# Kernel optimization log

Measured on AMD Instinct MI355X. Metric: run time of the kernel, lower is better.

## Reference

```python
import jax, jax.numpy as jnp
import numpy as np

NV = 6890   # SMPL vertex count (hard-coded in module)
NF = 13776  # SMPL face count
BATCH = 64


def _make_laplacian():
    # Mirrors LaplacianLoss.__init__: symmetric -1 adjacency from triangle
    # faces, diagonal = vertex degree, each row normalized by diag + 1e-8.
    rng = np.random.default_rng(0)
    faces = rng.integers(0, NV, size=(NF, 3))
    L = np.zeros((NV, NV), dtype=np.float32)
    L[faces[:, 0], faces[:, 1]] = -1
    L[faces[:, 1], faces[:, 0]] = -1
    L[faces[:, 1], faces[:, 2]] = -1
    L[faces[:, 2], faces[:, 1]] = -1
    L[faces[:, 2], faces[:, 0]] = -1
    L[faces[:, 0], faces[:, 2]] = -1
    r, c = np.diag_indices(NV)
    L[r, c] = -L.sum(1)
    L = L / (np.diag(L)[:, None] + 1e-8)
    return jnp.asarray(L)


def setup_inputs() -> dict:
    key = jax.random.key(0)
    x = jax.random.normal(key, (BATCH, NV, 3), dtype=jnp.float32)
    laplacian = _make_laplacian()
    return {"x": x, "laplacian": laplacian}


def reference(x, laplacian):
    # Dense Laplacian applied per batch: [v,w] x [b,w,d] -> [b,v,d]
    lx = jnp.einsum('vw,bwd->bvd', laplacian, x)
    # Squared norm over coordinate dim, then mean over (batch, vertices)
    # (average=False branch of the original module).
    return jnp.mean(jnp.sum(lx * lx, axis=2))
```

## Files before the change

kernel.cpp:

```cpp
#include <hip/hip_runtime.h>

#define NV    6890
#define NB    64
#define NCOL  192
#define CAP_W 256
#define MAIN4 1722
#define NIT   14
#define SCALE (1.0f / (64.0f * 6890.0f))

__global__ __launch_bounds__(256) void transpose_x_kernel(
    const float* __restrict__ x, float* __restrict__ Xt) {
  int i = blockIdx.x * blockDim.x + threadIdx.x;
  const int total = NB * NV * 3;
  if (i >= total) return;
  int d = i % 3;
  int w = (i / 3) % NV;
  int b = i / (3 * NV);
  Xt[(size_t)w * NCOL + b * 3 + d] = x[i];
}

template <bool USE_XT, bool USE_PARTIALS>
__global__ __launch_bounds__(256) void lap_rows_wave_kernel(
    const float* __restrict__ L,
    const float* __restrict__ X,
    float* __restrict__ partials,
    float* __restrict__ out_atomic) {
  const int lane = threadIdx.x & 63;
  const int wv   = threadIdx.x >> 6;
  const int v    = blockIdx.x * 4 + wv;
  if (v >= NV) return;

  __shared__ float4 s_c4[4][CAP_W];
  __shared__ int    s_cb[4][CAP_W];
  float4* __restrict__ sc4 = s_c4[wv];
  int*    __restrict__ scb = s_cb[wv];

  const float* __restrict__ row = L + (size_t)v * NV;
  const int head     = (v & 1) ? 2 : 0;
  const int extraPos = head ? 0 : (NV - 2);
  const float4* __restrict__ m4 = (const float4*)(row + head);

  const unsigned long long lmask = (1ull << lane) - 1ull;

  const int n0 = lane, n1 = lane + 64, n2 = lane + 128;
  const size_t o0 = (size_t)(n0 / 3) * (NV * 3) + (n0 % 3);
  const size_t o1 = (size_t)(n1 / 3) * (NV * 3) + (n1 % 3);
  const size_t o2 = (size_t)(n2 / 3) * (NV * 3) + (n2 % 3);

  float a0 = 0.f, a1 = 0.f, a2 = 0.f;
  int nnz = 0;

  auto gather3 = [&](float val, int col) {
    if (USE_XT) {
      const float* __restrict__ xr = X + (size_t)col * NCOL;
      a0 = fmaf(val, xr[n0], a0);
      a1 = fmaf(val, xr[n1], a1);
      a2 = fmaf(val, xr[n2], a2);
    } else {
      const size_t cb = (size_t)col * 3;
      a0 = fmaf(val, X[cb + o0], a0);
      a1 = fmaf(val, X[cb + o1], a1);
      a2 = fmaf(val, X[cb + o2], a2);
    }
  };

  auto apply = [&](int count) {
    for (int j = 0; j < count; ++j) {
      float4 f = sc4[j];
      int    cb = scb[j];
      if (f.x != 0.f) gather3(f.x, cb);
      if (f.y != 0.f) gather3(f.y, cb + 1);
      if (f.z != 0.f) gather3(f.z, cb + 2);
      if (f.w != 0.f) gather3(f.w, cb + 3);
    }
  };

  auto push_chunk = [&](bool nz, float4 f, int colbase) {
    unsigned long long m = __ballot(nz);
    if (nz) {
      int pos = nnz + __popcll(m & lmask);
      sc4[pos] = f;
      scb[pos] = colbase;
    }
    nnz += __popcll(m);
  };

  {
    const bool act = lane < 2;
    const int  col = extraPos + lane;
    float val = act ? row[col] : 0.f;
    push_chunk(val != 0.f, make_float4(val, 0.f, 0.f, 0.f), col);
  }

  for (int it = 0; it < NIT; ++it) {
    const int i0 = it * 128 + lane;
    const int i1 = i0 + 64;
    float4 f0 = make_float4(0.f, 0.f, 0.f, 0.f);
    float4 f1 = make_float4(0.f, 0.f, 0.f, 0.f);
    if (i0 < MAIN4) f0 = m4[i0];
    if (i1 < MAIN4) f1 = m4[i1];
    const bool nz0 = (f0.x != 0.f) | (f0.y != 0.f) | (f0.z != 0.f) | (f0.w != 0.f);
    const bool nz1 = (f1.x != 0.f) | (f1.y != 0.f) | (f1.z != 0.f) | (f1.w != 0.f);
    push_chunk(nz0, f0, head + i0 * 4);
    push_chunk(nz1, f1, head + i1 * 4);
    if (nnz > CAP_W - 130) { apply(nnz); nnz = 0; }
  }
  apply(nnz);

  float sq = fmaf(a0, a0, fmaf(a1, a1, a2 * a2));
  #pragma unroll
  for (int o = 32; o > 0; o >>= 1) sq += __shfl_down(sq, o);
  if (lane == 0) {
    if (USE_PARTIALS) partials[v] = sq;
    else              atomicAdd(out_atomic, sq * SCALE);
  }
}

__global__ __launch_bounds__(256) void reduce_kernel(
    const float* __restrict__ p, float* __restrict__ out) {
  int tid = threadIdx.x;
  float a = 0.0f;
  for (int i = tid; i < NV; i += 256) a += p[i];
  #pragma unroll
  for (int o = 32; o > 0; o >>= 1) a += __shfl_down(a, o);
  __shared__ float s_w[4];
  if ((tid & 63) == 0) s_w[tid >> 6] = a;
  __syncthreads();
  if (tid == 0) out[0] = (s_w[0] + s_w[1] + s_w[2] + s_w[3]) * SCALE;
}

__global__ void zero_out_kernel(float* p) {
  if (threadIdx.x == 0 && blockIdx.x == 0) p[0] = 0.0f;
}

extern "C" void kernel_launch(void* const* d_in, const int* in_sizes, int n_in,
                              void* d_out, int out_size, void* d_ws, size_t ws_size,
                              hipStream_t stream) {
  const float* x = (const float*)d_in[0];
  const float* L = (const float*)d_in[1];
  float* out = (float*)d_out;

  const size_t xt_bytes   = (size_t)NV * NCOL * sizeof(float);
  const size_t part_bytes = (size_t)NV * sizeof(float);
  const int grid = (NV + 3) / 4;

  if (ws_size >= xt_bytes + part_bytes) {
    float* Xt       = (float*)d_ws;
    float* partials = (float*)((char*)d_ws + xt_bytes);
    const int total = NB * NV * 3;
    transpose_x_kernel<<<(total + 255) / 256, 256, 0, stream>>>(x, Xt);
    lap_rows_wave_kernel<true, true><<<grid, 256, 0, stream>>>(L, Xt, partials, nullptr);
    reduce_kernel<<<1, 256, 0, stream>>>(partials, out);
  } else if (ws_size >= part_bytes) {
    float* partials = (float*)d_ws;
    lap_rows_wave_kernel<false, true><<<grid, 256, 0, stream>>>(L, x, partials, nullptr);
    reduce_kernel<<<1, 256, 0, stream>>>(partials, out);
  } else {
    zero_out_kernel<<<1, 64, 0, stream>>>(out);
    lap_rows_wave_kernel<false, false><<<grid, 256, 0, stream>>>(L, x, nullptr, out);
  }
}
```

Before: 63.04 us.

## Replace LDS nonzero compaction with ballot/readlane gathers and prefetch next row chunk

The per-wave shared-memory compaction of nonzero Laplacian entries is replaced by per-component ballots: each set bit is walked with ctz, and the value is broadcast with readlane before gathering the X row. The next float4 chunks of the row are software-prefetched one iteration ahead. The transpose kernel is reindexed so its writes are contiguous and its reads are gathered. This removes LDS traffic and the batch flush logic, but issues up to eight serialized ballot loops per iteration.

```diff
diff --git a/kernel.cpp b/kernel.cpp
--- a/kernel.cpp
+++ b/kernel.cpp
@@ -3,7 +3,6 @@
 #define NV    6890
 #define NB    64
 #define NCOL  192
-#define CAP_W 256
 #define MAIN4 1722
 #define NIT   14
 #define SCALE (1.0f / (64.0f * 6890.0f))
@@ -11,12 +10,13 @@
 __global__ __launch_bounds__(256) void transpose_x_kernel(
     const float* __restrict__ x, float* __restrict__ Xt) {
   int i = blockIdx.x * blockDim.x + threadIdx.x;
-  const int total = NB * NV * 3;
+  const int total = NV * NCOL;
   if (i >= total) return;
-  int d = i % 3;
-  int w = (i / 3) % NV;
-  int b = i / (3 * NV);
-  Xt[(size_t)w * NCOL + b * 3 + d] = x[i];
+  int n = i % NCOL;
+  int w = i / NCOL;
+  int b = n / 3;
+  int d = n % 3;
+  Xt[i] = x[(size_t)b * (NV * 3) + (size_t)w * 3 + d];
 }
 
 template <bool USE_XT, bool USE_PARTIALS>
@@ -30,17 +30,10 @@
   const int v    = blockIdx.x * 4 + wv;
   if (v >= NV) return;
 
-  __shared__ float4 s_c4[4][CAP_W];
-  __shared__ int    s_cb[4][CAP_W];
-  float4* __restrict__ sc4 = s_c4[wv];
-  int*    __restrict__ scb = s_cb[wv];
-
   const float* __restrict__ row = L + (size_t)v * NV;
   const int head     = (v & 1) ? 2 : 0;
   const int extraPos = head ? 0 : (NV - 2);
   const float4* __restrict__ m4 = (const float4*)(row + head);
-
-  const unsigned long long lmask = (1ull << lane) - 1ull;
 
   const int n0 = lane, n1 = lane + 64, n2 = lane + 128;
   const size_t o0 = (size_t)(n0 / 3) * (NV * 3) + (n0 % 3);
@@ -48,64 +41,69 @@
   const size_t o2 = (size_t)(n2 / 3) * (NV * 3) + (n2 % 3);
 
   float a0 = 0.f, a1 = 0.f, a2 = 0.f;
-  int nnz = 0;
 
-  auto gather3 = [&](float val, int col) {
-    if (USE_XT) {
-      const float* __restrict__ xr = X + (size_t)col * NCOL;
-      a0 = fmaf(val, xr[n0], a0);
-      a1 = fmaf(val, xr[n1], a1);
-      a2 = fmaf(val, xr[n2], a2);
-    } else {
-      const size_t cb = (size_t)col * 3;
-      a0 = fmaf(val, X[cb + o0], a0);
-      a1 = fmaf(val, X[cb + o1], a1);
-      a2 = fmaf(val, X[cb + o2], a2);
+  auto proc = [&](unsigned long long m, float src, int col0, int stride) {
+    while (m) {
+      const int s = (int)__builtin_ctzll(m);
+      m &= m - 1;
+      const float val =
+          __int_as_float(__builtin_amdgcn_readlane(__float_as_int(src), s));
+      const int col = col0 + s * stride;
+      if (USE_XT) {
+        const float* __restrict__ xr = X + (size_t)col * NCOL;
+        a0 = fmaf(val, xr[n0], a0);
+        a1 = fmaf(val, xr[n1], a1);
+        a2 = fmaf(val, xr[n2], a2);
+      } else {
+        const size_t cb = (size_t)col * 3;
+        a0 = fmaf(val, X[cb + o0], a0);
+        a1 = fmaf(val, X[cb + o1], a1);
+        a2 = fmaf(val, X[cb + o2], a2);
+      }
     }
-  };
-
-  auto apply = [&](int count) {
-    for (int j = 0; j < count; ++j) {
-      float4 f = sc4[j];
-      int    cb = scb[j];
-      if (f.x != 0.f) gather3(f.x, cb);
-      if (f.y != 0.f) gather3(f.y, cb + 1);
-      if (f.z != 0.f) gather3(f.z, cb + 2);
-      if (f.w != 0.f) gather3(f.w, cb + 3);
-    }
-  };
-
-  auto push_chunk = [&](bool nz, float4 f, int colbase) {
-    unsigned long long m = __ballot(nz);
-    if (nz) {
-      int pos = nnz + __popcll(m & lmask);
-      sc4[pos] = f;
-      scb[pos] = colbase;
-    }
-    nnz += __popcll(m);
   };
 
   {
     const bool act = lane < 2;
-    const int  col = extraPos + lane;
-    float val = act ? row[col] : 0.f;
-    push_chunk(val != 0.f, make_float4(val, 0.f, 0.f, 0.f), col);
+    const float val = act ? row[extraPos + lane] : 0.f;
+    proc(__ballot(act && val != 0.f), val, extraPos, 1);
   }
 
+  float4 c0 = m4[lane];
+  float4 c1 = m4[lane + 64];
   for (int it = 0; it < NIT; ++it) {
     const int i0 = it * 128 + lane;
     const int i1 = i0 + 64;
-    float4 f0 = make_float4(0.f, 0.f, 0.f, 0.f);
-    float4 f1 = make_float4(0.f, 0.f, 0.f, 0.f);
-    if (i0 < MAIN4) f0 = m4[i0];
-    if (i1 < MAIN4) f1 = m4[i1];
-    const bool nz0 = (f0.x != 0.f) | (f0.y != 0.f) | (f0.z != 0.f) | (f0.w != 0.f);
-    const bool nz1 = (f1.x != 0.f) | (f1.y != 0.f) | (f1.z != 0.f) | (f1.w != 0.f);
-    push_chunk(nz0, f0, head + i0 * 4);
-    push_chunk(nz1, f1, head + i1 * 4);
-    if (nnz > CAP_W - 130) { apply(nnz); nnz = 0; }
+    const int j0 = min(i0 + 128, MAIN4 - 1);
+    const int j1 = min(i1 + 128, MAIN4 - 1);
+    const float4 p0 = m4[j0];
+    const float4 p1 = m4[j1];
+
+    const bool act0 = i0 < MAIN4;
+    const bool act1 = i1 < MAIN4;
+    const unsigned long long mx0 = __ballot(act0 && c0.x != 0.f);
+    const unsigned long long my0 = __ballot(act0 && c0.y != 0.f);
+    const unsigned long long mz0 = __ballot(act0 && c0.z != 0.f);
+    const unsigned long long mw0 = __ballot(act0 && c0.w != 0.f);
+    const unsigned long long mx1 = __ballot(act1 && c1.x != 0.f);
+    const unsigned long long my1 = __ballot(act1 && c1.y != 0.f);
+    const unsigned long long mz1 = __ballot(act1 && c1.z != 0.f);
+    const unsigned long long mw1 = __ballot(act1 && c1.w != 0.f);
+
+    const int base0 = head + it * 512;
+    const int base1 = base0 + 256;
+    proc(mx0, c0.x, base0 + 0, 4);
+    proc(my0, c0.y, base0 + 1, 4);
+    proc(mz0, c0.z, base0 + 2, 4);
+    proc(mw0, c0.w, base0 + 3, 4);
+    proc(mx1, c1.x, base1 + 0, 4);
+    proc(my1, c1.y, base1 + 1, 4);
+    proc(mz1, c1.z, base1 + 2, 4);
+    proc(mw1, c1.w, base1 + 3, 4);
+
+    c0 = p0;
+    c1 = p1;
   }
-  apply(nnz);
 
   float sq = fmaf(a0, a0, fmaf(a1, a1, a2 * a2));
   #pragma unroll
@@ -147,7 +145,7 @@
   if (ws_size >= xt_bytes + part_bytes) {
     float* Xt       = (float*)d_ws;
     float* partials = (float*)((char*)d_ws + xt_bytes);
-    const int total = NB * NV * 3;
+    const int total = NV * NCOL;
     transpose_x_kernel<<<(total + 255) / 256, 256, 0, stream>>>(x, Xt);
     lap_rows_wave_kernel<true, true><<<grid, 256, 0, stream>>>(L, Xt, partials, nullptr);
     reduce_kernel<<<1, 256, 0, stream>>>(partials, out);
```

Measured after the change: 58.05 us. 7.9% less time.
